# Performance work log

Hardware: AMD Instinct MI355X
Metric: run time of the kernel (lower is better)

The kernel has to match this reference:

```python
import jax, jax.numpy as jnp
import numpy as np

N, T, C = 4096, 365, 32
ALPHAS = (1.0 / 3.0, 1.0 / 3.0, 1.0 / 3.0)


def setup_inputs() -> dict:
    key = jax.random.key(0)
    k1, k2, k3 = jax.random.split(key, 3)
    raw = jax.random.normal(k1, (N, T, C), dtype=jnp.float32)
    log_class_probabilities = jax.nn.log_softmax(raw, axis=-1)  # valid log-probs
    labels = jax.random.randint(k2, (N,), 0, C, dtype=jnp.int32)
    y_true = jnp.broadcast_to(labels[:, None], (N, T))  # constant label per sample
    # sequence 'time remaining': counts down to 0; first zero marks stopping time t_final
    lengths = jax.random.randint(k3, (N,), T // 2, T + 1, dtype=jnp.int32)  # in [T/2, T]
    t_idx = jnp.arange(T, dtype=jnp.int32)
    timestamps_left = jnp.maximum(lengths[:, None] - 1 - t_idx[None, :], 0).astype(jnp.float32)
    return {
        "log_class_probabilities": log_class_probabilities,
        "timestamps_left": timestamps_left,
        "y_true": y_true,
    }


def reference(log_class_probabilities, timestamps_left, y_true):
    a0, a1, a2 = ALPHAS
    n, t_len, c = log_class_probabilities.shape
    dtype = log_class_probabilities.dtype
    Tf = jnp.asarray(t_len, dtype)

    # NLLLoss(reduction='none'): ce[n,t] = -logp[n,t,y[n,t]]
    lp_true = jnp.take_along_axis(log_class_probabilities, y_true[..., None].astype(jnp.int32), axis=2)[..., 0]
    cross_entropy = -lp_true  # (N, T)
    classification_loss = cross_entropy.mean(0)  # (T,)

    # earliness reward: p(correct class) * (1 - t/T) * (1 - timestamps_left/T), summed over t, mean over n
    t_grid = jnp.arange(t_len, dtype=dtype)
    p_correct = jnp.exp(lp_true)  # (N, T)
    earliness_reward = (p_correct * (1.0 - t_grid / Tf) * (1.0 - timestamps_left / Tf)).sum(1).mean(0)

    # proximity reward: sum over classes c, pairs i<j in class c of
    #   exp(lp_i[tf_i]) * exp(lp_j[tf_j]) * ((tf_i - tf_j)/T)^2
    # Vectorized via per-class moments: sum_{i<j} e_i e_j (tf_i - tf_j)^2 = A*D - B^2
    # with A = sum e, B = sum e*tf, D = sum e*tf^2 (segment sums over class labels).
    t_final = jnp.argmax(timestamps_left == 0, axis=1)  # (N,)
    labels = y_true[:, 0].astype(jnp.int32)  # (N,) constant per row
    lp_tf = jnp.take_along_axis(log_class_probabilities, t_final[:, None, None], axis=1)[:, 0, :]  # (N, C)
    e = jnp.exp(jnp.take_along_axis(lp_tf, labels[:, None], axis=1)[:, 0])  # (N,)
    tf = t_final.astype(dtype)
    A = jax.ops.segment_sum(e, labels, num_segments=c)
    B = jax.ops.segment_sum(e * tf, labels, num_segments=c)
    D = jax.ops.segment_sum(e * tf * tf, labels, num_segments=c)
    proximity = jnp.sum(A * D - B * B) / (Tf * Tf)

    loss = a0 * classification_loss - a1 * earliness_reward - a2 * proximity  # (T,)
    return loss
```

## Files before the change

kernel.cpp:

```cpp
#include <hip/hip_runtime.h>

#define NN 4096
#define TT 365
#define CC 32
#define RPB 8
#define BLOCK 512
#define F4_PER_ROW (TT * CC / 4)

#define WS_DOUBLES (TT + 1 + 3 * CC)

__global__ __launch_bounds__(BLOCK) void stp_main(
    const float4* __restrict__ logp4,
    const float* __restrict__ tl,
    const int* __restrict__ yt,
    double* __restrict__ ws)
{
    __shared__ float  s_cls[TT];
    __shared__ double s_red[BLOCK / 64];
    __shared__ int    s_label[RPB];
    __shared__ float  s_tf[RPB];

    const int tid = threadIdx.x;
    const int n0 = blockIdx.x * RPB;

    for (int i = tid; i < TT; i += BLOCK) s_cls[i] = 0.0f;
    if (tid < RPB) {
        const size_t base = (size_t)(n0 + tid) * TT;
        s_label[tid] = yt[base];
        s_tf[tid]    = tl[base];
    }
    __syncthreads();

    double earl = 0.0;
    const float invT = 1.0f / 365.0f;

    for (int r = 0; r < RPB; ++r) {
        const int   label = s_label[r];
        const float tf_f  = s_tf[r];
        const int   j0    = label >> 2;
        const int   c0    = label & 3;
        const float4* row = logp4 + (size_t)(n0 + r) * F4_PER_ROW;

        for (int i = tid; i < F4_PER_ROW; i += BLOCK) {
            const float4 v = row[i];
            if ((i & 7) == j0) {
                const int t = i >> 3;
                const float lp = (c0 & 2) ? ((c0 & 1) ? v.w : v.z)
                                          : ((c0 & 1) ? v.y : v.x);
                atomicAdd(&s_cls[t], -lp);
                const float pc  = expf(lp);
                const float tlv = fmaxf(tf_f - (float)t, 0.0f);
                earl += (double)(pc * (1.0f - (float)t * invT)
                                    * (1.0f - tlv * invT));
                if ((float)t == tf_f) {
                    const double e   = (double)pc;
                    const double tfd = (double)t;
                    atomicAdd(&ws[TT + 1 + label],           e);
                    atomicAdd(&ws[TT + 1 + CC + label],      e * tfd);
                    atomicAdd(&ws[TT + 1 + 2 * CC + label],  e * tfd * tfd);
                }
            }
        }
    }

    for (int off = 32; off > 0; off >>= 1)
        earl += __shfl_down(earl, off, 64);
    if ((tid & 63) == 0) s_red[tid >> 6] = earl;
    __syncthreads();
    if (tid == 0) {
        double s = 0.0;
        #pragma unroll
        for (int w = 0; w < BLOCK / 64; ++w) s += s_red[w];
        atomicAdd(&ws[TT], s);
    }

    for (int i = tid; i < TT; i += BLOCK)
        atomicAdd(&ws[i], (double)s_cls[i]);
}

__global__ __launch_bounds__(BLOCK) void stp_finalize(
    const double* __restrict__ ws, float* __restrict__ out)
{
    __shared__ double s_scalar;
    const int tid = threadIdx.x;
    if (tid == 0) {
        double p = 0.0;
        #pragma unroll
        for (int c = 0; c < CC; ++c) {
            const double A = ws[TT + 1 + c];
            const double B = ws[TT + 1 + CC + c];
            const double D = ws[TT + 1 + 2 * CC + c];
            p += A * D - B * B;
        }
        p /= (365.0 * 365.0);
        const double e = ws[TT] / (double)NN;
        s_scalar = (1.0 / 3.0) * (e + p);
    }
    __syncthreads();
    if (tid < TT) {
        const double cls = ws[tid] / (double)NN;
        out[tid] = (float)((1.0 / 3.0) * cls - s_scalar);
    }
}

extern "C" void kernel_launch(void* const* d_in, const int* in_sizes, int n_in,
                              void* d_out, int out_size, void* d_ws, size_t ws_size,
                              hipStream_t stream)
{
    const float4* logp4 = (const float4*)d_in[0];
    const float*  tl    = (const float*)d_in[1];
    const int*    yt    = (const int*)d_in[2];
    float* out = (float*)d_out;
    double* ws = (double*)d_ws;

    hipMemsetAsync(ws, 0, WS_DOUBLES * sizeof(double), stream);
    stp_main<<<NN / RPB, BLOCK, 0, stream>>>(logp4, tl, yt, ws);
    stp_finalize<<<1, BLOCK, 0, stream>>>(ws, out);
}
```

Measured before the change: 53.79 us.

## Interleave loads across eight rows and replace shared atomics with slot writes

The row loop and the column loop swap places, so each thread issues eight independent float4 loads, one per row, before any compute. The aim is more memory requests in flight in this bandwidth-bound kernel. Shared-memory atomicAdd per timestep is replaced by one plain write into an 8×T slot array, summed once at the end, which removes LDS atomic contention. Block size halves to 256 and the finalize kernel now loops over the output. The cost is higher register pressure from holding eight float4 values per thread.

```diff
diff --git a/kernel.cpp b/kernel.cpp
--- a/kernel.cpp
+++ b/kernel.cpp
@@ -4,63 +4,72 @@
 #define TT 365
 #define CC 32
 #define RPB 8
-#define BLOCK 512
+#define BLOCK 256
+#define GRID (NN / RPB)
 #define F4_PER_ROW (TT * CC / 4)
 
 #define WS_DOUBLES (TT + 1 + 3 * CC)
 
 __global__ __launch_bounds__(BLOCK) void stp_main(
-    const float4* __restrict__ logp4,
+    const float* __restrict__ logp,
     const float* __restrict__ tl,
-    const int* __restrict__ yt,
+    const int*  __restrict__ yt,
     double* __restrict__ ws)
 {
-    __shared__ float  s_cls[TT];
+    __shared__ float  s_cls[8][TT + 7];
     __shared__ double s_red[BLOCK / 64];
-    __shared__ int    s_label[RPB];
-    __shared__ float  s_tf[RPB];
 
     const int tid = threadIdx.x;
-    const int n0 = blockIdx.x * RPB;
+    const int n0  = blockIdx.x * RPB;
 
-    for (int i = tid; i < TT; i += BLOCK) s_cls[i] = 0.0f;
-    if (tid < RPB) {
-        const size_t base = (size_t)(n0 + tid) * TT;
-        s_label[tid] = yt[base];
-        s_tf[tid]    = tl[base];
+    int   lab[RPB], j0[RPB], comp[RPB];
+    float tff[RPB];
+    const float* rowp[RPB];
+    #pragma unroll
+    for (int r = 0; r < RPB; ++r) {
+        const size_t rb = (size_t)(n0 + r) * TT;
+        lab[r]  = yt[rb];
+        tff[r]  = tl[rb];
+        j0[r]   = lab[r] >> 2;
+        comp[r] = lab[r] & 3;
+        rowp[r] = logp + rb * CC;
     }
-    __syncthreads();
 
     double earl = 0.0;
     const float invT = 1.0f / 365.0f;
 
-    for (int r = 0; r < RPB; ++r) {
-        const int   label = s_label[r];
-        const float tf_f  = s_tf[r];
-        const int   j0    = label >> 2;
-        const int   c0    = label & 3;
-        const float4* row = logp4 + (size_t)(n0 + r) * F4_PER_ROW;
+    for (int i = tid; i < F4_PER_ROW; i += BLOCK) {
+        float4 v[RPB];
+        #pragma unroll
+        for (int r = 0; r < RPB; ++r)
+            v[r] = *(const float4*)(rowp[r] + (size_t)i * 4);
 
-        for (int i = tid; i < F4_PER_ROW; i += BLOCK) {
-            const float4 v = row[i];
-            if ((i & 7) == j0) {
-                const int t = i >> 3;
-                const float lp = (c0 & 2) ? ((c0 & 1) ? v.w : v.z)
-                                          : ((c0 & 1) ? v.y : v.x);
-                atomicAdd(&s_cls[t], -lp);
+        const int   j  = i & 7;
+        const int   t  = i >> 3;
+        const float tF = (float)t;
+        const float wt = 1.0f - tF * invT;
+
+        float acc = 0.0f;
+        #pragma unroll
+        for (int r = 0; r < RPB; ++r) {
+            if (j == j0[r]) {
+                const int   c  = comp[r];
+                const float lp = c == 0 ? v[r].x : c == 1 ? v[r].y
+                               : c == 2 ? v[r].z : v[r].w;
+                acc -= lp;
                 const float pc  = expf(lp);
-                const float tlv = fmaxf(tf_f - (float)t, 0.0f);
-                earl += (double)(pc * (1.0f - (float)t * invT)
-                                    * (1.0f - tlv * invT));
-                if ((float)t == tf_f) {
+                const float tlv = fmaxf(tff[r] - tF, 0.0f);
+                earl += (double)(pc * wt * (1.0f - tlv * invT));
+                if (tF == tff[r]) {
                     const double e   = (double)pc;
-                    const double tfd = (double)t;
-                    atomicAdd(&ws[TT + 1 + label],           e);
-                    atomicAdd(&ws[TT + 1 + CC + label],      e * tfd);
-                    atomicAdd(&ws[TT + 1 + 2 * CC + label],  e * tfd * tfd);
+                    const double tfd = (double)tF;
+                    atomicAdd(&ws[TT + 1 + lab[r]],          e);
+                    atomicAdd(&ws[TT + 1 + CC + lab[r]],     e * tfd);
+                    atomicAdd(&ws[TT + 1 + 2 * CC + lab[r]], e * tfd * tfd);
                 }
             }
         }
+        s_cls[j][t] = acc;
     }
 
     for (int off = 32; off > 0; off >>= 1)
@@ -74,8 +83,12 @@
         atomicAdd(&ws[TT], s);
     }
 
-    for (int i = tid; i < TT; i += BLOCK)
-        atomicAdd(&ws[i], (double)s_cls[i]);
+    for (int i = tid; i < TT; i += BLOCK) {
+        float s = 0.0f;
+        #pragma unroll
+        for (int jj = 0; jj < 8; ++jj) s += s_cls[jj][i];
+        atomicAdd(&ws[i], (double)s);
+    }
 }
 
 __global__ __launch_bounds__(BLOCK) void stp_finalize(
@@ -97,9 +110,9 @@
         s_scalar = (1.0 / 3.0) * (e + p);
     }
     __syncthreads();
-    if (tid < TT) {
-        const double cls = ws[tid] / (double)NN;
-        out[tid] = (float)((1.0 / 3.0) * cls - s_scalar);
+    for (int i = tid; i < TT; i += BLOCK) {
+        const double cls = ws[i] / (double)NN;
+        out[i] = (float)((1.0 / 3.0) * cls - s_scalar);
     }
 }
 
@@ -107,13 +120,13 @@
                               void* d_out, int out_size, void* d_ws, size_t ws_size,
                               hipStream_t stream)
 {
-    const float4* logp4 = (const float4*)d_in[0];
-    const float*  tl    = (const float*)d_in[1];
-    const int*    yt    = (const int*)d_in[2];
+    const float* logp = (const float*)d_in[0];
+    const float* tl   = (const float*)d_in[1];
+    const int*   yt   = (const int*)d_in[2];
     float* out = (float*)d_out;
     double* ws = (double*)d_ws;
 
     hipMemsetAsync(ws, 0, WS_DOUBLES * sizeof(double), stream);
-    stp_main<<<NN / RPB, BLOCK, 0, stream>>>(logp4, tl, yt, ws);
+    stp_main<<<GRID, BLOCK, 0, stream>>>(logp, tl, yt, ws);
     stp_finalize<<<1, BLOCK, 0, stream>>>(ws, out);
 }
```

Result: slower. 58.59 us (+8.9%).
